# Kernel optimization log

Measured on AMD Instinct MI355X. Metric: run time of the kernel, lower is better.

Reference implementation:

```python
import jax, jax.numpy as jnp
import numpy as np

NU, NI, E = 20000, 8000, 64
DV, DT = 4096, 768
NE, B = 200000, 4096
L_HET, L_HOMO = 2, 1
K_ISG, K_UCG = 10, 20
MMW, WD = 0.1, 1e-4


def setup_inputs() -> dict:
    ks = jax.random.split(jax.random.key(0), 14)
    return {
        "feat_v": jax.random.normal(ks[0], (NI, DV), jnp.float32),
        "feat_t": jax.random.normal(ks[1], (NI, DT), jnp.float32),
        "pref_v": jax.random.normal(ks[2], (NU, E), jnp.float32) * 0.1,
        "pref_t": jax.random.normal(ks[3], (NU, E), jnp.float32) * 0.1,
        "W_v": jax.random.normal(ks[4], (DV, E), jnp.float32) * 0.02,
        "W_t": jax.random.normal(ks[5], (DT, E), jnp.float32) * 0.02,
        "user_v_alpha": jax.random.normal(ks[6], (1,), jnp.float32),
        "user_nb_weights": jax.random.normal(ks[7], (NU, K_UCG), jnp.float32),
        "edge_users": jax.random.randint(ks[8], (NE,), 0, NU, jnp.int32),
        "edge_items": jax.random.randint(ks[9], (NE,), 0, NI, jnp.int32),
        "u_ids": jax.random.randint(ks[10], (B,), 0, NU, jnp.int32),
        "pos_ids": jax.random.randint(ks[11], (B,), 0, NI, jnp.int32),
        "neg_ids": jax.random.randint(ks[12], (B,), 0, NI, jnp.int32),
        "user_nb": jax.random.randint(ks[13], (NU, K_UCG), 0, NU, jnp.int32),
    }


def reference(feat_v, feat_t, pref_v, pref_t, W_v, W_t, user_v_alpha,
              user_nb_weights, edge_users, edge_items, u_ids, pos_ids,
              neg_ids, user_nb):
    N = NU + NI
    # bidirectional bipartite edges (items offset by NU)
    src = jnp.concatenate([edge_users, edge_items + NU])
    dst = jnp.concatenate([edge_items + NU, edge_users])
    deg = jax.ops.segment_sum(jnp.ones_like(src, jnp.float32), dst, num_segments=N)
    deg = jnp.maximum(deg, 1.0)
    norm = (1.0 / jnp.sqrt(deg[src] * deg[dst]))[:, None]

    def hetero_gcn(feat, pref, W):
        x = jnp.concatenate([pref, feat @ W], axis=0)  # [N, E]
        h, out = x, x
        for _ in range(L_HET):
            h = jax.ops.segment_sum(h[src] * norm, dst, num_segments=N)
            out = out + h
        return out[:NU], out[NU:]

    u_v, i_v = hetero_gcn(feat_v, pref_v, W_v)
    u_t, i_t = hetero_gcn(feat_t, pref_t, W_t)
    a_v = jax.nn.sigmoid(user_v_alpha[0])
    u_f = jnp.concatenate([a_v * u_v, (1.0 - a_v) * u_t], axis=1)  # [NU, 2E]
    i_f = jnp.concatenate([i_v, i_t], axis=1)                      # [NI, 2E]

    # Item Semantic Graph: KNN over cosine sim, no grad through adjacency.
    def knn_adj(f):
        fn = f / jnp.linalg.norm(f, axis=-1, keepdims=True)
        sim = fn @ fn.T                       # [NI, NI]
        _, idx = jax.lax.top_k(sim, K_ISG)
        return jnp.zeros((NI, NI), f.dtype).at[jnp.arange(NI)[:, None], idx].set(1.0)

    adj = jax.lax.stop_gradient(MMW * knn_adj(feat_v) + (1.0 - MMW) * knn_adj(feat_t))
    rs = adj.sum(axis=1)
    adj = adj * jnp.where(rs > 0, 1.0 / rs, 0.0)[:, None]

    h_i = i_f
    for _ in range(L_HOMO):
        h_i = adj @ h_i

    # User Co-occurrence Graph: scatter-softmax attention aggregation, vectorized.
    attn = jax.nn.softmax(user_nb_weights, axis=1)  # [NU, K]
    h_u = u_f
    for _ in range(L_HOMO):
        h_u = jnp.einsum('uk,ukd->ud', attn, h_u[user_nb])

    z_u = u_f + h_u
    z_i = i_f + h_i
    pos = jnp.sum(z_u[u_ids] * z_i[pos_ids], axis=1)
    neg = jnp.sum(z_u[u_ids] * z_i[neg_ids], axis=1)
    bpr = -jnp.mean(jax.nn.log_sigmoid(pos - neg))
    reg = WD * (jnp.sum(pref_v ** 2) + jnp.sum(pref_t ** 2) + user_v_alpha[0] ** 2) / 2.0
    return bpr + reg
```

## Files before the change

### kernel.cpp

```cpp
#include <hip/hip_runtime.h>
#include <cstdint>
#include <cstddef>

#define NU_C   20000
#define NI_C   8000
#define NTOT_C 28000
#define NE_C   200000
#define B_C    4096
#define NPAD_C 8064
#define NCHUNK 63
#define NPAIR  2016

typedef unsigned short u16;
typedef unsigned int   u32;
typedef unsigned char  u8;
typedef __bf16 bf16x8 __attribute__((ext_vector_type(8)));
typedef float  f32x4  __attribute__((ext_vector_type(4)));

static __device__ __forceinline__ u16 f2bf(float f) {
  u32 u = __float_as_uint(f);
  return (u16)((u + 0x7fffu + ((u >> 16) & 1u)) >> 16);
}

static __device__ __forceinline__ void gl_lds16(const void* g, void* l) {
  __builtin_amdgcn_global_load_lds(
      (const __attribute__((address_space(1))) void*)g,
      (__attribute__((address_space(3))) void*)l, 16, 0, 0);
}

static __device__ __forceinline__ int xcd_swz(int b) {
  return (b & 7) * (NPAIR / 8) + (b >> 3);
}

__global__ void conv_kernel2(const float* __restrict__ Fv, const float* __restrict__ Ft,
                             u16* __restrict__ Fbv, u16* __restrict__ Fbt,
                             u8* __restrict__ Fv8,
                             float* __restrict__ rnv, float* __restrict__ rnt,
                             const float* __restrict__ pv, const float* __restrict__ pt,
                             float* __restrict__ x2) {
  int b = blockIdx.x;
  const int tid = threadIdx.x;
  float ss = 0.f;
  if (b < NPAD_C) {
    const int row = b;
    u16* dst  = Fbv + (size_t)row * 4096;
    u8*  dst8 = Fv8 + (size_t)row * 4096;
    if (row < NI_C) {
      const float* src = Fv + (size_t)row * 4096;
      for (int c = tid * 4; c < 4096; c += 1024) {
        float4 f = *(const float4*)(src + c);
        ss += f.x*f.x + f.y*f.y + f.z*f.z + f.w*f.w;
        ushort4 v; v.x = f2bf(f.x); v.y = f2bf(f.y); v.z = f2bf(f.z); v.w = f2bf(f.w);
        *(ushort4*)(dst + c) = v;
        int w8 = __builtin_amdgcn_cvt_pk_fp8_f32(f.x, f.y, 0, false);
        w8 = __builtin_amdgcn_cvt_pk_fp8_f32(f.z, f.w, w8, true);
        *(u32*)(dst8 + c) = (u32)w8;
      }
    } else {
      for (int c = tid * 4; c < 4096; c += 1024) {
        ushort4 v; v.x = v.y = v.z = v.w = 0;
        *(ushort4*)(dst + c) = v;
        *(u32*)(dst8 + c) = 0u;
      }
    }
    #pragma unroll
    for (int off = 32; off; off >>= 1) ss += __shfl_xor(ss, off);
    __shared__ float red[4];
    if ((tid & 63) == 0) red[tid >> 6] = ss;
    __syncthreads();
    if (tid == 0) {
      float s = red[0] + red[1] + red[2] + red[3];
      rnv[row] = (row < NI_C) ? rsqrtf(s) : 0.f;
    }
  } else if (b < 2 * NPAD_C) {
    const int row = b - NPAD_C;
    u16* dst = Fbt + (size_t)row * 768;
    if (row < NI_C) {
      const float* src = Ft + (size_t)row * 768;
      for (int c = tid * 4; c < 768; c += 1024) {
        float4 f = *(const float4*)(src + c);
        ss += f.x*f.x + f.y*f.y + f.z*f.z + f.w*f.w;
        ushort4 v; v.x = f2bf(f.x); v.y = f2bf(f.y); v.z = f2bf(f.z); v.w = f2bf(f.w);
        *(ushort4*)(dst + c) = v;
      }
    } else {
      for (int c = tid * 4; c < 768; c += 1024) {
        ushort4 v; v.x = v.y = v.z = v.w = 0;
        *(ushort4*)(dst + c) = v;
      }
    }
    #pragma unroll
    for (int off = 32; off; off >>= 1) ss += __shfl_xor(ss, off);
    __shared__ float red[4];
    if ((tid & 63) == 0) red[tid >> 6] = ss;
    __syncthreads();
    if (tid == 0) {
      float s = red[0] + red[1] + red[2] + red[3];
      rnt[row] = (row < NI_C) ? rsqrtf(s) : 0.f;
    }
  } else {
    const int b2 = b - 2 * NPAD_C;
    #pragma unroll
    for (int k = 0; k < 8; ++k) {
      int gid = b2 * 2048 + k * 256 + tid;
      int u = gid >> 7, c = gid & 127;
      x2[gid] = (c < 64) ? pv[(size_t)u * 64 + c] : pt[(size_t)u * 64 + (c - 64)];
    }
  }
}

static __device__ __forceinline__ void simtopk_fp8_body(
    int bid, char* smem, const u8* __restrict__ F, const float* __restrict__ rn,
    u32* __restrict__ tv) {
  u8*    sB   = (u8*)smem;
  u8*    sA   = (u8*)(smem + 16384);
  float* T    = (float*)smem;
  int*   mk   = (int*)smem;
  int*   mk2  = (int*)(smem + 20480);
  float* sRNI = (float*)(smem + 33792);
  float* sRNJ = (float*)(smem + 34304);

  const int tid  = threadIdx.x;
  const int lane = tid & 63;
  const int wv   = tid >> 6;
  const int n15  = lane & 15;
  const int quad = lane >> 4;

  int I = 0, rem = xcd_swz(bid);
  { int rowlen = NCHUNK;
    while (rem >= rowlen) { rem -= rowlen; rowlen--; I++; } }
  const int J = I + rem;

  const int l2   = lane >> 2;
  const int lseg = (lane & 3) ^ (l2 & 3) ^ (lane >> 4);
  const u8* gB[2]; const u8* gA[2]; u8* lB[2]; u8* lA[2];
  #pragma unroll
  for (int rep = 0; rep < 2; ++rep) {
    int row = wv * 32 + rep * 16 + l2;
    gB[rep] = F + (size_t)(I * 128 + row) * 4096 + lseg * 16;
    gA[rep] = F + (size_t)(J * 128 + row) * 4096 + lseg * 16;
    lB[rep] = sB + (wv * 32 + rep * 16) * 64;
    lA[rep] = sA + (wv * 32 + rep * 16) * 64;
  }
  const int s_n = (n15 & 3) ^ (n15 >> 2);
  const int q2  = quad >> 1;
  const int q8  = (quad & 1) * 8;
  const int rB0 = (wv * 32 + n15) * 64;
  const int rB1 = rB0 + 16 * 64;

  f32x4 acc[2][8];
  #pragma unroll
  for (int tf = 0; tf < 2; ++tf)
    #pragma unroll
    for (int af = 0; af < 8; ++af) { f32x4 z = {0.f,0.f,0.f,0.f}; acc[tf][af] = z; }

  for (int k0 = 0; k0 < 4096; k0 += 128) {
    __syncthreads();
    gl_lds16(gB[0] + k0,      lB[0]);
    gl_lds16(gB[0] + k0 + 64, lB[0] + 8192);
    gl_lds16(gB[1] + k0,      lB[1]);
    gl_lds16(gB[1] + k0 + 64, lB[1] + 8192);
    gl_lds16(gA[0] + k0,      lA[0]);
    gl_lds16(gA[0] + k0 + 64, lA[0] + 8192);
    gl_lds16(gA[1] + k0,      lA[1]);
    gl_lds16(gA[1] + k0 + 64, lA[1] + 8192);
    if (k0 == 0) {
      if (tid < 128) sRNJ[tid] = rn[J * 128 + tid];
      else           sRNI[tid - 128] = rn[I * 128 + (tid - 128)];
    }
    __syncthreads();
    #pragma unroll
    for (int ksub = 0; ksub < 2; ++ksub) {
      const u8* bBase = sB + ksub * 8192;
      const u8* aBase = sA + ksub * 8192;
      #pragma unroll
      for (int ks = 0; ks < 2; ++ks) {
        const int sw = (((ks * 2 + q2) ^ s_n) << 4) + q8;
        long long b0 = *(const long long*)(bBase + rB0 + sw);
        long long b1 = *(const long long*)(bBase + rB1 + sw);
        #pragma unroll
        for (int af = 0; af < 8; ++af) {
          long long a = *(const long long*)(aBase + (af * 16 + n15) * 64 + sw);
          acc[0][af] = __builtin_amdgcn_mfma_f32_16x16x32_fp8_fp8(a, b0, acc[0][af], 0, 0, 0);
          acc[1][af] = __builtin_amdgcn_mfma_f32_16x16x32_fp8_fp8(a, b1, acc[1][af], 0, 0, 0);
        }
      }
    }
  }

  int bk[2][10];
  #pragma unroll
  for (int tf = 0; tf < 2; ++tf)
    #pragma unroll
    for (int j = 0; j < 10; ++j) bk[tf][j] = 0;

  #pragma unroll
  for (int af = 0; af < 8; ++af) {
    const float4 rn4 = *(const float4*)(sRNJ + af * 16 + quad * 4);
    const float rna[4] = {rn4.x, rn4.y, rn4.z, rn4.w};
    #pragma unroll
    for (int r = 0; r < 4; ++r) {
      const int ci = J * 128 + af * 16 + quad * 4 + r;
      #pragma unroll
      for (int tf = 0; tf < 2; ++tf) {
        float v = acc[tf][af][r] * rna[r];
        int key = (int)((__float_as_uint(v) & 0xFFFFE000u) | (u32)ci);
        if (ci < NI_C && key > bk[tf][9]) {
          bk[tf][9] = key;
          #pragma unroll
          for (int j = 9; j > 0; --j)
            if (bk[tf][j] > bk[tf][j-1]) { int t = bk[tf][j]; bk[tf][j] = bk[tf][j-1]; bk[tf][j-1] = t; }
        }
      }
    }
  }
  __syncthreads();
  #pragma unroll
  for (int tf = 0; tf < 2; ++tf) {
    int rl = wv * 32 + tf * 16 + n15;
    #pragma unroll
    for (int j = 0; j < 10; ++j) mk[rl * 40 + quad * 10 + j] = bk[tf][j];
  }
  __syncthreads();
  if (tid < 128) {
    int* m = mk + tid * 40;
    int h0 = 0, h1 = 10, h2 = 20, h3 = 30;
    int v0 = m[0], v1 = m[10], v2 = m[20], v3 = m[30];
    #pragma unroll
    for (int s = 0; s < 10; ++s) {
      int m01 = v0 > v1 ? v0 : v1, m23 = v2 > v3 ? v2 : v3;
      int mx = m01 > m23 ? m01 : m23;
      mk2[tid * 10 + s] = mx;
      if      (mx == v0) { ++h0; v0 = (h0 < 10) ? m[h0] : (int)0x80000000; }
      else if (mx == v1) { ++h1; v1 = (h1 < 20) ? m[h1] : (int)0x80000000; }
      else if (mx == v2) { ++h2; v2 = (h2 < 30) ? m[h2] : (int)0x80000000; }
      else               { ++h3; v3 = (h3 < 40) ? m[h3] : (int)0x80000000; }
    }
  }
  __syncthreads();
  { u32* o = tv + ((size_t)J * NPAD_C + I * 128) * 10;
    for (int g = tid; g < 1280; g += 256) o[g] = (u32)mk2[g]; }

  if (I == J) return;

  int bj[2][10];
  #pragma unroll
  for (int s = 0; s < 2; ++s)
    #pragma unroll
    for (int j = 0; j < 10; ++j) bj[s][j] = 0;

  #pragma unroll
  for (int tf = 0; tf < 2; ++tf) {
    __syncthreads();
    #pragma unroll
    for (int af = 0; af < 8; ++af)
      #pragma unroll
      for (int r = 0; r < 4; ++r)
        T[(af * 16 + quad * 4 + r) * 66 + wv * 16 + n15] = acc[tf][af][r];
    __syncthreads();
    #pragma unroll
    for (int s = 0; s < 2; ++s) {
      const int c_own = wv * 32 + s * 16 + n15;
      #pragma unroll
      for (int j = 0; j < 16; ++j) {
        const int t  = quad * 32 + tf * 16 + j;
        const int t64 = quad * 16 + j;
        float v = T[c_own * 66 + t64] * sRNI[t];
        const int ti = I * 128 + t;
        int key = (int)((__float_as_uint(v) & 0xFFFFE000u) | (u32)ti);
        if (ti < NI_C && key > bj[s][9]) {
          bj[s][9] = key;
          #pragma unroll
          for (int q = 9; q > 0; --q)
            if (bj[s][q] > bj[s][q-1]) { int tt = bj[s][q]; bj[s][q] = bj[s][q-1]; bj[s][q-1] = tt; }
        }
      }
    }
  }
  __syncthreads();
  #pragma unroll
  for (int s = 0; s < 2; ++s) {
    int rl = wv * 32 + s * 16 + n15;
    #pragma unroll
    for (int j = 0; j < 10; ++j) mk[rl * 40 + quad * 10 + j] = bj[s][j];
  }
  __syncthreads();
  if (tid < 128) {
    int* m = mk + tid * 40;
    int h0 = 0, h1 = 10, h2 = 20, h3 = 30;
    int v0 = m[0], v1 = m[10], v2 = m[20], v3 = m[30];
    #pragma unroll
    for (int s = 0; s < 10; ++s) {
      int m01 = v0 > v1 ? v0 : v1, m23 = v2 > v3 ? v2 : v3;
      int mx = m01 > m23 ? m01 : m23;
      mk2[tid * 10 + s] = mx;
      if      (mx == v0) { ++h0; v0 = (h0 < 10) ? m[h0] : (int)0x80000000; }
      else if (mx == v1) { ++h1; v1 = (h1 < 20) ? m[h1] : (int)0x80000000; }
      else if (mx == v2) { ++h2; v2 = (h2 < 30) ? m[h2] : (int)0x80000000; }
      else               { ++h3; v3 = (h3 < 40) ? m[h3] : (int)0x80000000; }
    }
  }
  __syncthreads();
  { u32* o = tv + ((size_t)I * NPAD_C + J * 128) * 10;
    for (int g = tid; g < 1280; g += 256) o[g] = (u32)mk2[g]; }
}

static __device__ __forceinline__ void simtopk_bf16_body(
    int bid, char* smem, const u16* __restrict__ F, const float* __restrict__ rn,
    u32* __restrict__ tv) {
  u16*   sB   = (u16*)smem;
  u16*   sA   = (u16*)(smem + 16384);
  float* T    = (float*)smem;
  int*   mk   = (int*)smem;
  int*   mk2  = (int*)(smem + 20480);
  float* sRNI = (float*)(smem + 34816);
  float* sRNJ = (float*)(smem + 35328);

  const int tid  = threadIdx.x;
  const int lane = tid & 63;
  const int wv   = tid >> 6;
  const int n15  = lane & 15;
  const int quad = lane >> 4;

  int I = 0, rem = xcd_swz(bid);
  { int rowlen = NCHUNK;
    while (rem >= rowlen) { rem -= rowlen; rowlen--; I++; } }
  const int J = I + rem;

  const int l8  = lane >> 3;
  const int sgu = ((lane & 7) ^ l8) << 3;
  const u16* gB[4]; const u16* gA[4]; u16* lB[4]; u16* lA[4];
  #pragma unroll
  for (int rep = 0; rep < 4; ++rep) {
    int row = wv * 32 + rep * 8 + l8;
    gB[rep] = F + (size_t)(I * 128 + row) * 768 + sgu;
    gA[rep] = F + (size_t)(J * 128 + row) * 768 + sgu;
    lB[rep] = sB + wv * 2048 + rep * 512;
    lA[rep] = sA + wv * 2048 + rep * 512;
  }
  const int swu0 = ((quad    ) ^ (n15 & 7)) << 3;
  const int swu1 = ((quad + 4) ^ (n15 & 7)) << 3;
  const int rowB0 = (wv * 32 + n15) * 64;
  const int rowB1 = rowB0 + 16 * 64;

  f32x4 acc[2][8];
  #pragma unroll
  for (int tf = 0; tf < 2; ++tf)
    #pragma unroll
    for (int af = 0; af < 8; ++af) { f32x4 z = {0.f,0.f,0.f,0.f}; acc[tf][af] = z; }

  for (int k0 = 0; k0 < 768; k0 += 64) {
    __syncthreads();
    #pragma unroll
    for (int rep = 0; rep < 4; ++rep) gl_lds16(gB[rep] + k0, lB[rep]);
    #pragma unroll
    for (int rep = 0; rep < 4; ++rep) gl_lds16(gA[rep] + k0, lA[rep]);
    if (k0 == 0) {
      if (tid < 128) sRNJ[tid] = rn[J * 128 + tid];
      else           sRNI[tid - 128] = rn[I * 128 + (tid - 128)];
    }
    __syncthreads();
    #pragma unroll
    for (int ks = 0; ks < 2; ++ks) {
      const int swu = ks ? swu1 : swu0;
      bf16x8 b0 = *(const bf16x8*)(sB + rowB0 + swu);
      bf16x8 b1 = *(const bf16x8*)(sB + rowB1 + swu);
      #pragma unroll
      for (int af = 0; af < 8; ++af) {
        bf16x8 a = *(const bf16x8*)(sA + (af * 16 + n15) * 64 + swu);
        acc[0][af] = __builtin_amdgcn_mfma_f32_16x16x32_bf16(a, b0, acc[0][af], 0, 0, 0);
        acc[1][af] = __builtin_amdgcn_mfma_f32_16x16x32_bf16(a, b1, acc[1][af], 0, 0, 0);
      }
    }
  }

  int bk[2][10];
  #pragma unroll
  for (int tf = 0; tf < 2; ++tf)
    #pragma unroll
    for (int j = 0; j < 10; ++j) bk[tf][j] = 0;

  #pragma unroll
  for (int af = 0; af < 8; ++af) {
    const float4 rn4 = *(const float4*)(sRNJ + af * 16 + quad * 4);
    const float rna[4] = {rn4.x, rn4.y, rn4.z, rn4.w};
    #pragma unroll
    for (int r = 0; r < 4; ++r) {
      const int ci = J * 128 + af * 16 + quad * 4 + r;
      #pragma unroll
      for (int tf = 0; tf < 2; ++tf) {
        float v = acc[tf][af][r] * rna[r];
        int key = (int)((__float_as_uint(v) & 0xFFFFE000u) | (u32)ci);
        if (ci < NI_C && key > bk[tf][9]) {
          bk[tf][9] = key;
          #pragma unroll
          for (int j = 9; j > 0; --j)
            if (bk[tf][j] > bk[tf][j-1]) { int t = bk[tf][j]; bk[tf][j] = bk[tf][j-1]; bk[tf][j-1] = t; }
        }
      }
    }
  }
  __syncthreads();
  #pragma unroll
  for (int tf = 0; tf < 2; ++tf) {
    int rl = wv * 32 + tf * 16 + n15;
    #pragma unroll
    for (int j = 0; j < 10; ++j) mk[rl * 40 + quad * 10 + j] = bk[tf][j];
  }
  __syncthreads();
  if (tid < 128) {
    int* m = mk + tid * 40;
    int h0 = 0, h1 = 10, h2 = 20, h3 = 30;
    int v0 = m[0], v1 = m[10], v2 = m[20], v3 = m[30];
    #pragma unroll
    for (int s = 0; s < 10; ++s) {
      int m01 = v0 > v1 ? v0 : v1, m23 = v2 > v3 ? v2 : v3;
      int mx = m01 > m23 ? m01 : m23;
      mk2[tid * 10 + s] = mx;
      if      (mx == v0) { ++h0; v0 = (h0 < 10) ? m[h0] : (int)0x80000000; }
      else if (mx == v1) { ++h1; v1 = (h1 < 20) ? m[h1] : (int)0x80000000; }
      else if (mx == v2) { ++h2; v2 = (h2 < 30) ? m[h2] : (int)0x80000000; }
      else               { ++h3; v3 = (h3 < 40) ? m[h3] : (int)0x80000000; }
    }
  }
  __syncthreads();
  { u32* o = tv + ((size_t)J * NPAD_C + I * 128) * 10;
    for (int g = tid; g < 1280; g += 256) o[g] = (u32)mk2[g]; }

  if (I == J) return;

  int bj[2][10];
  #pragma unroll
  for (int s = 0; s < 2; ++s)
    #pragma unroll
    for (int j = 0; j < 10; ++j) bj[s][j] = 0;

  #pragma unroll
  for (int tf = 0; tf < 2; ++tf) {
    __syncthreads();
    #pragma unroll
    for (int af = 0; af < 8; ++af)
      #pragma unroll
      for (int r = 0; r < 4; ++r)
        T[(af * 16 + quad * 4 + r) * 66 + wv * 16 + n15] = acc[tf][af][r];
    __syncthreads();
    #pragma unroll
    for (int s = 0; s < 2; ++s) {
      const int c_own = wv * 32 + s * 16 + n15;
      #pragma unroll
      for (int j = 0; j < 16; ++j) {
        const int t  = quad * 32 + tf * 16 + j;
        const int t64 = quad * 16 + j;
        float v = T[c_own * 66 + t64] * sRNI[t];
        const int ti = I * 128 + t;
        int key = (int)((__float_as_uint(v) & 0xFFFFE000u) | (u32)ti);
        if (ti < NI_C && key > bj[s][9]) {
          bj[s][9] = key;
          #pragma unroll
          for (int q = 9; q > 0; --q)
            if (bj[s][q] > bj[s][q-1]) { int tt = bj[s][q]; bj[s][q] = bj[s][q-1]; bj[s][q-1] = tt; }
        }
      }
    }
  }
  __syncthreads();
  #pragma unroll
  for (int s = 0; s < 2; ++s) {
    int rl = wv * 32 + s * 16 + n15;
    #pragma unroll
    for (int j = 0; j < 10; ++j) mk[rl * 40 + quad * 10 + j] = bj[s][j];
  }
  __syncthreads();
  if (tid < 128) {
    int* m = mk + tid * 40;
    int h0 = 0, h1 = 10, h2 = 20, h3 = 30;
    int v0 = m[0], v1 = m[10], v2 = m[20], v3 = m[30];
    #pragma unroll
    for (int s = 0; s < 10; ++s) {
      int m01 = v0 > v1 ? v0 : v1, m23 = v2 > v3 ? v2 : v3;
      int mx = m01 > m23 ? m01 : m23;
      mk2[tid * 10 + s] = mx;
      if      (mx == v0) { ++h0; v0 = (h0 < 10) ? m[h0] : (int)0x80000000; }
      else if (mx == v1) { ++h1; v1 = (h1 < 20) ? m[h1] : (int)0x80000000; }
      else if (mx == v2) { ++h2; v2 = (h2 < 30) ? m[h2] : (int)0x80000000; }
      else               { ++h3; v3 = (h3 < 40) ? m[h3] : (int)0x80000000; }
    }
  }
  __syncthreads();
  { u32* o = tv + ((size_t)I * NPAD_C + J * 128) * 10;
    for (int g = tid; g < 1280; g += 256) o[g] = (u32)mk2[g]; }
}

static __device__ __forceinline__ void merge4_body(int mb, int* fkbase,
                                                   const u32* __restrict__ tv,
                                                   int* __restrict__ idx) {
  const int w    = threadIdx.x >> 6;
  const int lane = threadIdx.x & 63;
  const int row  = mb * 4 + w;
  int* fk = fkbase + w * 640;
  for (int g = lane; g < 630; g += 64)
    fk[g] = (int)tv[((size_t)(g / 10) * NPAD_C + row) * 10 + (g % 10)];
  if (lane < 10) fk[630 + lane] = (int)0x80000000;
  __syncthreads();
  int v[10];
  #pragma unroll
  for (int j = 0; j < 10; ++j) v[j] = fk[lane + j * 64];
  #pragma unroll 1
  for (int s = 0; s < 10; ++s) {
    int loc = v[0];
    #pragma unroll
    for (int j = 1; j < 10; ++j) loc = v[j] > loc ? v[j] : loc;
    #pragma unroll
    for (int off = 32; off; off >>= 1) {
      int o = __shfl_xor(loc, off); loc = o > loc ? o : loc;
    }
    if (lane == 0) idx[row * 10 + s] = loc & 0x1FFF;
    #pragma unroll
    for (int j = 0; j < 10; ++j) if (v[j] == loc) v[j] = (int)0x80000000;
  }
}

__launch_bounds__(256)
__global__ void merge4_kernel(const u32* __restrict__ tv, int* __restrict__ idx) {
  __shared__ int fk[4 * 640];
  merge4_body(blockIdx.x, fk, tv, idx);
}

template<int D>
static __device__ __forceinline__ void gemm_xw_body(
    int bid, char* smem, const u16* __restrict__ F, const u16* __restrict__ Wt,
    float* __restrict__ x2, int modeoff) {
  u16* sF = (u16*)smem;
  const int tid  = threadIdx.x;
  const int lane = tid & 63;
  const int wv   = tid >> 6;
  const int n15  = lane & 15;
  const int quad = lane >> 4;
  const int l8   = lane >> 3;
  const int sgu  = ((lane & 7) ^ l8) << 3;
  const u16* gF[2]; u16* lF[2];
  #pragma unroll
  for (int rep = 0; rep < 2; ++rep) {
    int row = rep * 32 + wv * 8 + l8;
    gF[rep] = F + (size_t)(bid * 64 + row) * D + sgu;
    lF[rep] = sF + (rep * 32 + wv * 8) * 64;
  }
  const int swu0 = ((quad    ) ^ (n15 & 7)) << 3;
  const int swu1 = ((quad + 4) ^ (n15 & 7)) << 3;

  f32x4 acc[4];
  #pragma unroll
  for (int nf = 0; nf < 4; ++nf) { f32x4 z = {0.f,0.f,0.f,0.f}; acc[nf] = z; }

  for (int k0 = 0; k0 < D; k0 += 64) {
    __syncthreads();
    gl_lds16(gF[0] + k0, lF[0]);
    gl_lds16(gF[1] + k0, lF[1]);
    __syncthreads();
    #pragma unroll
    for (int ks = 0; ks < 2; ++ks) {
      const int swu = ks ? swu1 : swu0;
      bf16x8 a = *(const bf16x8*)(sF + (wv * 16 + n15) * 64 + swu);
      #pragma unroll
      for (int nf = 0; nf < 4; ++nf) {
        bf16x8 b = *(const bf16x8*)(Wt + (size_t)(nf * 16 + n15) * D + k0 + ks * 32 + quad * 8);
        acc[nf] = __builtin_amdgcn_mfma_f32_16x16x32_bf16(a, b, acc[nf], 0, 0, 0);
      }
    }
  }
  #pragma unroll
  for (int nf = 0; nf < 4; ++nf)
    #pragma unroll
    for (int r = 0; r < 4; ++r) {
      int row = bid * 64 + wv * 16 + quad * 4 + r;
      if (row < NI_C)
        x2[(size_t)(NU_C + row) * 128 + modeoff + nf * 16 + n15] = acc[nf][r];
    }
}

static __device__ __forceinline__ void gather2_body(
    int bid, const int* __restrict__ row_start, const int* __restrict__ esrc,
    const float* __restrict__ ew, const float* __restrict__ x2, float* __restrict__ h1) {
  const int node = bid * 2 + (threadIdx.x >> 7);
  const int ch   = threadIdx.x & 127;
  if (node >= NTOT_C) return;
  const int b = row_start[node], e = row_start[node + 1];
  float acc = 0.f;
  for (int i = b; i < e; ++i)
    acc += ew[i] * x2[(size_t)esrc[i] * 128 + ch];
  h1[(size_t)node * 128 + ch] = acc;
}

static __device__ __forceinline__ void gather_comb2_body(
    int bid, const int* __restrict__ row_start, const int* __restrict__ esrc,
    const float* __restrict__ ew, const float* __restrict__ x2,
    const float* __restrict__ h1, const float* __restrict__ alpha,
    float* __restrict__ uf, float* __restrict__ ifb) {
  const int node = bid * 2 + (threadIdx.x >> 7);
  const int ch   = threadIdx.x & 127;
  if (node >= NTOT_C) return;
  const int b = row_start[node], e = row_start[node + 1];
  float acc = 0.f;
  for (int i = b; i < e; ++i)
    acc += ew[i] * h1[(size_t)esrc[i] * 128 + ch];
  float val = x2[(size_t)node * 128 + ch] + h1[(size_t)node * 128 + ch] + acc;
  if (node < NU_C) {
    float av = 1.f / (1.f + expf(-alpha[0]));
    float coef = (ch < 64) ? av : (1.f - av);
    uf[(size_t)node * 128 + ch] = coef * val;
  } else {
    ifb[(size_t)(node - NU_C) * 128 + ch] = val;
  }
}

__launch_bounds__(256)
__global__ void fusedA_kernel(const u8* __restrict__ F8, const float* __restrict__ rnv,
                              u32* __restrict__ tv,
                              const u16* __restrict__ Fvb, const u16* __restrict__ Wtv,
                              const u16* __restrict__ Ftb, const u16* __restrict__ Wtt,
                              float* __restrict__ x2) {
  __shared__ __align__(16) char smem[34816];
  int b = blockIdx.x;
  if (b < 125) { gemm_xw_body<4096>(b, smem, Fvb, Wtv, x2, 0); return; }
  b -= 125;
  if (b < 125) { gemm_xw_body<768>(b, smem, Ftb, Wtt, x2, 64); return; }
  simtopk_fp8_body(b - 125, smem, F8, rnv, tv);
}

__launch_bounds__(256)
__global__ void fusedB_kernel(const int* __restrict__ row_start, const int* __restrict__ esrc,
                              const float* __restrict__ ew, const float* __restrict__ x2,
                              float* __restrict__ h1,
                              const u32* __restrict__ tv, int* __restrict__ idx) {
  __shared__ int fk[4 * 640];
  int b = blockIdx.x;
  if (b < 2000) { merge4_body(b, fk, tv, idx); return; }
  gather2_body(b - 2000, row_start, esrc, ew, x2, h1);
}

__launch_bounds__(256)
__global__ void fusedC_kernel(const u16* __restrict__ Ftb, const float* __restrict__ rnt,
                              u32* __restrict__ tv2,
                              const int* __restrict__ row_start, const int* __restrict__ esrc,
                              const float* __restrict__ ew, const float* __restrict__ x2,
                              const float* __restrict__ h1, const float* __restrict__ alpha,
                              float* __restrict__ uf, float* __restrict__ ifb) {
  __shared__ __align__(16) char smem[40960];
  int b = blockIdx.x;
  if (b < NPAIR) { simtopk_bf16_body(b, smem, Ftb, rnt, tv2); return; }
  gather_comb2_body(b - NPAIR, row_start, esrc, ew, x2, h1, alpha, uf, ifb);
}

__global__ void deg_count_kernel(const int* __restrict__ eu, const int* __restrict__ ei,
                                 float* deg) {
  int e = blockIdx.x * 256 + threadIdx.x;
  if (e < NE_C) {
    atomicAdd(&deg[eu[e]], 1.f);
    atomicAdd(&deg[NU_C + ei[e]], 1.f);
  }
}

__global__ void scan_kernel(float* __restrict__ deg, int* __restrict__ row_start,
                            int* __restrict__ cursor) {
  __shared__ int part[1024];
  const int tid = threadIdx.x;
  const int base = tid * 28;
  float dl[28];
  int local[28];
  int s = 0;
  #pragma unroll
  for (int j = 0; j < 28; ++j) {
    int n = base + j;
    float df = (n < NTOT_C) ? deg[n] : 0.f;
    dl[j] = df;
    local[j] = s; s += (int)df;
  }
  part[tid] = s;
  __syncthreads();
  for (int off = 1; off < 1024; off <<= 1) {
    int v = (tid >= off) ? part[tid - off] : 0;
    __syncthreads();
    part[tid] += v;
    __syncthreads();
  }
  int pre = (tid > 0) ? part[tid - 1] : 0;
  #pragma unroll
  for (int j = 0; j < 28; ++j) {
    int n = base + j;
    if (n < NTOT_C) {
      row_start[n] = pre + local[j];
      cursor[n]    = pre + local[j];
      deg[n]       = rsqrtf(fmaxf(dl[j], 1.f));
    }
  }
  if (tid == 1023) row_start[NTOT_C] = part[1023];
}

__global__ void place_kernel(const int* __restrict__ eu, const int* __restrict__ ei,
                             const float* __restrict__ dinv, int* __restrict__ cursor,
                             int* __restrict__ esrc, float* __restrict__ ew) {
  int e = blockIdx.x * 256 + threadIdx.x;
  if (e >= NE_C) return;
  int u = eu[e], v = NU_C + ei[e];
  float w = dinv[u] * dinv[v];
  int p1 = atomicAdd(&cursor[v], 1);  esrc[p1] = u; ew[p1] = w;
  int p2 = atomicAdd(&cursor[u], 1);  esrc[p2] = v; ew[p2] = w;
}

__global__ void wtrans_kernel(const float* __restrict__ Wv, const float* __restrict__ Wti,
                              u16* __restrict__ Ov, u16* __restrict__ Ot) {
  __shared__ u16 sT[64][72];
  int b = blockIdx.x;
  const float* W; u16* O; int D;
  if (b < 64) { W = Wv; O = Ov; D = 4096; }
  else        { b -= 64; W = Wti; O = Ot; D = 768; }
  const int k0 = b * 64;
  const int r = threadIdx.x >> 6;
  const int c = threadIdx.x & 63;
  for (int rr = r; rr < 64; rr += 4)
    sT[c][rr] = f2bf(W[(size_t)(k0 + rr) * 64 + c]);
  __syncthreads();
  const int n = threadIdx.x >> 2, seg = threadIdx.x & 3;
  uint4 a0 = *(const uint4*)&sT[n][seg * 16];
  uint4 a1 = *(const uint4*)&sT[n][seg * 16 + 8];
  *(uint4*)(O + (size_t)n * D + k0 + seg * 16)     = a0;
  *(uint4*)(O + (size_t)n * D + k0 + seg * 16 + 8) = a1;
}

__global__ void zuzi_kernel(const float* __restrict__ uf, const float* __restrict__ w,
                            const int* __restrict__ nb, const float* __restrict__ ifb,
                            const int* __restrict__ iv, const int* __restrict__ it,
                            float* __restrict__ zu, float* __restrict__ zi) {
  const int c = threadIdx.x;
  if (blockIdx.x < NU_C) {
    const int u = blockIdx.x;
    __shared__ float at[20];
    if (c < 20) at[c] = w[u * 20 + c];
    __syncthreads();
    float e[20]; float m = -1e30f;
    #pragma unroll
    for (int k = 0; k < 20; ++k) { e[k] = at[k]; m = fmaxf(m, e[k]); }
    float ssum = 0.f;
    #pragma unroll
    for (int k = 0; k < 20; ++k) { e[k] = expf(e[k] - m); ssum += e[k]; }
    float inv = 1.f / ssum;
    float acc = 0.f;
    #pragma unroll
    for (int k = 0; k < 20; ++k) {
      int j = nb[u * 20 + k];
      acc += e[k] * inv * uf[(size_t)j * 128 + c];
    }
    zu[(size_t)u * 128 + c] = uf[(size_t)u * 128 + c] + acc;
  } else {
    const int i = blockIdx.x - NU_C;
    float sv = 0.f, st = 0.f;
    #pragma unroll
    for (int k = 0; k < 10; ++k) sv += ifb[(size_t)iv[i * 10 + k] * 128 + c];
    #pragma unroll
    for (int k = 0; k < 10; ++k) st += ifb[(size_t)it[i * 10 + k] * 128 + c];
    zi[(size_t)i * 128 + c] = ifb[(size_t)i * 128 + c] + 0.01f * sv + 0.09f * st;
  }
}

__global__ void loss_kernel(const float* __restrict__ zu, const float* __restrict__ zi,
                            const int* __restrict__ uid, const int* __restrict__ pid,
                            const int* __restrict__ nid, const float* __restrict__ pv,
                            const float* __restrict__ pt, const float* __restrict__ alpha,
                            float* __restrict__ out) {
  if (blockIdx.x < 1024) {
    int wv = threadIdx.x >> 6, lane = threadIdx.x & 63;
    int b = blockIdx.x * 4 + wv;
    int u = uid[b], p = pid[b], n = nid[b];
    float2 a  = *(const float2*)(zu + (size_t)u * 128 + lane * 2);
    float2 xp = *(const float2*)(zi + (size_t)p * 128 + lane * 2);
    float2 xn = *(const float2*)(zi + (size_t)n * 128 + lane * 2);
    float d = a.x * (xp.x - xn.x) + a.y * (xp.y - xn.y);
    #pragma unroll
    for (int off = 32; off; off >>= 1) d += __shfl_xor(d, off);
    if (lane == 0) {
      float xv = -d;
      float sp = fmaxf(xv, 0.f) + log1pf(expf(-fabsf(xv)));
      atomicAdd(out, sp * (1.f / (float)B_C));
    }
  } else {
    const size_t N1 = (size_t)NU_C * 64;
    float acc = 0.f;
    for (size_t i = (size_t)(blockIdx.x - 1024) * 256 + threadIdx.x; i < 2 * N1;
         i += (size_t)512 * 256) {
      float x = (i < N1) ? pv[i] : pt[i - N1];
      acc += x * x;
    }
    #pragma unroll
    for (int off = 32; off; off >>= 1) acc += __shfl_xor(acc, off);
    __shared__ float red[4];
    if ((threadIdx.x & 63) == 0) red[threadIdx.x >> 6] = acc;
    __syncthreads();
    if (threadIdx.x == 0) {
      float s = red[0] + red[1] + red[2] + red[3];
      atomicAdd(out, 0.5e-4f * s);
    }
    if (blockIdx.x == 1024 && threadIdx.x == 0) {
      float a = alpha[0];
      atomicAdd(out, 0.5e-4f * a * a);
    }
  }
}

extern "C" void kernel_launch(void* const* d_in, const int* in_sizes, int n_in,
                              void* d_out, int out_size, void* d_ws, size_t ws_size,
                              hipStream_t stream) {
  const float* feat_v = (const float*)d_in[0];
  const float* feat_t = (const float*)d_in[1];
  const float* pref_v = (const float*)d_in[2];
  const float* pref_t = (const float*)d_in[3];
  const float* W_v    = (const float*)d_in[4];
  const float* W_t    = (const float*)d_in[5];
  const float* alpha  = (const float*)d_in[6];
  const float* unw    = (const float*)d_in[7];
  const int* eu       = (const int*)d_in[8];
  const int* ei       = (const int*)d_in[9];
  const int* u_ids    = (const int*)d_in[10];
  const int* pos_ids  = (const int*)d_in[11];
  const int* neg_ids  = (const int*)d_in[12];
  const int* user_nb  = (const int*)d_in[13];
  float* out = (float*)d_out;
  char* ws = (char*)d_ws;

  size_t off = 0;
  auto alloc = [&](size_t bytes) { char* p = ws + off; off += (bytes + 255) & ~(size_t)255; return p; };
  u16*   fvbf  = (u16*)alloc((size_t)NPAD_C * 4096 * 2);
  u8*    fv8   = (u8*)alloc((size_t)NPAD_C * 4096);
  u16*   ftbf  = (u16*)alloc((size_t)NPAD_C * 768 * 2);
  u16*   wtv   = (u16*)alloc((size_t)64 * 4096 * 2);
  u16*   wtt   = (u16*)alloc((size_t)64 * 768 * 2);
  float* rn_v  = (float*)alloc(NPAD_C * 4);
  float* rn_t  = (float*)alloc(NPAD_C * 4);
  int*   idx_v = (int*)alloc(NI_C * 10 * 4);
  int*   idx_t = (int*)alloc(NI_C * 10 * 4);
  float* dinv  = (float*)alloc(NTOT_C * 4);
  int*   rowst = (int*)alloc((NTOT_C + 1) * 4);
  int*   curs  = (int*)alloc(NTOT_C * 4);
  int*   esrc  = (int*)alloc((size_t)2 * NE_C * 4);
  float* ew    = (float*)alloc((size_t)2 * NE_C * 4);
  float* x2    = (float*)alloc((size_t)NTOT_C * 128 * 4);
  float* h1    = (float*)alloc((size_t)NTOT_C * 128 * 4);
  char*  pC    = alloc((size_t)(NU_C + NI_C) * 128 * 4 * 2);
  u32*   tvb   = (u32*)pC;
  u32*   tvb2  = (u32*)fvbf;
  float* u_f   = (float*)pC;
  float* i_f   = (float*)(pC + (size_t)NU_C * 128 * 4);
  float* z_u   = (float*)(pC + (size_t)(NU_C + NI_C) * 128 * 4);
  float* z_i   = (float*)(pC + (size_t)(2 * NU_C + NI_C) * 128 * 4);

  hipMemsetAsync(out, 0, sizeof(float), stream);
  hipMemsetAsync(dinv, 0, NTOT_C * 4, stream);

  deg_count_kernel<<<(NE_C + 255) / 256, 256, 0, stream>>>(eu, ei, dinv);
  scan_kernel<<<1, 1024, 0, stream>>>(dinv, rowst, curs);
  place_kernel<<<(NE_C + 255) / 256, 256, 0, stream>>>(eu, ei, dinv, curs, esrc, ew);
  conv_kernel2<<<2 * NPAD_C + 1250, 256, 0, stream>>>(feat_v, feat_t, fvbf, ftbf, fv8,
                                                      rn_v, rn_t, pref_v, pref_t, x2);
  wtrans_kernel<<<76, 256, 0, stream>>>(W_v, W_t, wtv, wtt);

  fusedA_kernel<<<250 + NPAIR, 256, 0, stream>>>(
      fv8, rn_v, tvb, fvbf, wtv, ftbf, wtt, x2);

  fusedB_kernel<<<2000 + 14000, 256, 0, stream>>>(rowst, esrc, ew, x2, h1, tvb, idx_v);

  fusedC_kernel<<<NPAIR + 14000, 256, 0, stream>>>(
      ftbf, rn_t, tvb2, rowst, esrc, ew, x2, h1, alpha, u_f, i_f);

  merge4_kernel<<<2000, 256, 0, stream>>>(tvb2, idx_t);
  zuzi_kernel<<<NU_C + NI_C, 128, 0, stream>>>(u_f, unw, user_nb, i_f, idx_v, idx_t, z_u, z_i);
  loss_kernel<<<1536, 256, 0, stream>>>(z_u, z_i, u_ids, pos_ids, neg_ids,
                                        pref_v, pref_t, alpha, out);
}
```

Before: 1.048 ms.

## Reschedule stages into fewer fused launches to overlap independent work

Folds degree counting and the weight transpose into the conversion kernel, and folds CSR placement into fusedA. The bf16 similarity top-k moves from fusedC up into fusedB, alongside the visual merge and the first gather. The text merge moves into fusedC, so the standalone merge kernel is removed. This cuts the number of kernel launches and lets independent stages share a grid to fill idle CUs. The cost is heavier multi-role kernels and more careful reasoning about buffer aliasing (tvb2 reuses the fvbf region) across the new stage order.

```diff
diff --git a/kernel.cpp b/kernel.cpp
--- a/kernel.cpp
+++ b/kernel.cpp
@@ -32,12 +32,36 @@
   return (b & 7) * (NPAIR / 8) + (b >> 3);
 }
 
+static __device__ __forceinline__ void wtrans_body(int b, const float* __restrict__ Wv,
+                                                   const float* __restrict__ Wti,
+                                                   u16* __restrict__ Ov, u16* __restrict__ Ot) {
+  __shared__ u16 sT[64][72];
+  const float* W; u16* O; int D;
+  if (b < 64) { W = Wv; O = Ov; D = 4096; }
+  else        { b -= 64; W = Wti; O = Ot; D = 768; }
+  const int k0 = b * 64;
+  const int r = threadIdx.x >> 6;
+  const int c = threadIdx.x & 63;
+  for (int rr = r; rr < 64; rr += 4)
+    sT[c][rr] = f2bf(W[(size_t)(k0 + rr) * 64 + c]);
+  __syncthreads();
+  const int n = threadIdx.x >> 2, seg = threadIdx.x & 3;
+  uint4 a0 = *(const uint4*)&sT[n][seg * 16];
+  uint4 a1 = *(const uint4*)&sT[n][seg * 16 + 8];
+  *(uint4*)(O + (size_t)n * D + k0 + seg * 16)     = a0;
+  *(uint4*)(O + (size_t)n * D + k0 + seg * 16 + 8) = a1;
+}
+
 __global__ void conv_kernel2(const float* __restrict__ Fv, const float* __restrict__ Ft,
                              u16* __restrict__ Fbv, u16* __restrict__ Fbt,
                              u8* __restrict__ Fv8,
                              float* __restrict__ rnv, float* __restrict__ rnt,
                              const float* __restrict__ pv, const float* __restrict__ pt,
-                             float* __restrict__ x2) {
+                             float* __restrict__ x2,
+                             const float* __restrict__ Wv, const float* __restrict__ Wti,
+                             u16* __restrict__ wtv, u16* __restrict__ wtt,
+                             const int* __restrict__ eu, const int* __restrict__ ei,
+                             float* __restrict__ deg) {
   int b = blockIdx.x;
   const int tid = threadIdx.x;
   float ss = 0.f;
@@ -98,13 +122,22 @@
       float s = red[0] + red[1] + red[2] + red[3];
       rnt[row] = (row < NI_C) ? rsqrtf(s) : 0.f;
     }
-  } else {
-    const int b2 = b - 2 * NPAD_C;
+  } else if (b < 2 * NPAD_C + 76) {
+    wtrans_body(b - 2 * NPAD_C, Wv, Wti, wtv, wtt);
+  } else if (b < 2 * NPAD_C + 76 + 1250) {
+    const int b2 = b - (2 * NPAD_C + 76);
     #pragma unroll
     for (int k = 0; k < 8; ++k) {
       int gid = b2 * 2048 + k * 256 + tid;
       int u = gid >> 7, c = gid & 127;
       x2[gid] = (c < 64) ? pv[(size_t)u * 64 + c] : pt[(size_t)u * 64 + (c - 64)];
+    }
+  } else {
+    const int b2 = b - (2 * NPAD_C + 76 + 1250);
+    int e = b2 * 256 + tid;
+    if (e < NE_C) {
+      atomicAdd(&deg[eu[e]], 1.f);
+      atomicAdd(&deg[NU_C + ei[e]], 1.f);
     }
   }
 }
@@ -518,12 +551,6 @@
     #pragma unroll
     for (int j = 0; j < 10; ++j) if (v[j] == loc) v[j] = (int)0x80000000;
   }
-}
-
-__launch_bounds__(256)
-__global__ void merge4_kernel(const u32* __restrict__ tv, int* __restrict__ idx) {
-  __shared__ int fk[4 * 640];
-  merge4_body(blockIdx.x, fk, tv, idx);
 }
 
 template<int D>
@@ -613,51 +640,62 @@
   }
 }
 
+static __device__ __forceinline__ void place_body(
+    int bid, const int* __restrict__ eu, const int* __restrict__ ei,
+    const float* __restrict__ dinv, int* __restrict__ cursor,
+    int* __restrict__ esrc, float* __restrict__ ew) {
+  int e = bid * 256 + threadIdx.x;
+  if (e >= NE_C) return;
+  int u = eu[e], v = NU_C + ei[e];
+  float w = dinv[u] * dinv[v];
+  int p1 = atomicAdd(&cursor[v], 1);  esrc[p1] = u; ew[p1] = w;
+  int p2 = atomicAdd(&cursor[u], 1);  esrc[p2] = v; ew[p2] = w;
+}
+
 __launch_bounds__(256)
 __global__ void fusedA_kernel(const u8* __restrict__ F8, const float* __restrict__ rnv,
                               u32* __restrict__ tv,
                               const u16* __restrict__ Fvb, const u16* __restrict__ Wtv,
                               const u16* __restrict__ Ftb, const u16* __restrict__ Wtt,
-                              float* __restrict__ x2) {
+                              float* __restrict__ x2,
+                              const int* __restrict__ eu, const int* __restrict__ ei,
+                              const float* __restrict__ dinv, int* __restrict__ cursor,
+                              int* __restrict__ esrc, float* __restrict__ ew) {
   __shared__ __align__(16) char smem[34816];
   int b = blockIdx.x;
   if (b < 125) { gemm_xw_body<4096>(b, smem, Fvb, Wtv, x2, 0); return; }
   b -= 125;
   if (b < 125) { gemm_xw_body<768>(b, smem, Ftb, Wtt, x2, 64); return; }
-  simtopk_fp8_body(b - 125, smem, F8, rnv, tv);
+  b -= 125;
+  if (b < NPAIR) { simtopk_fp8_body(b, smem, F8, rnv, tv); return; }
+  place_body(b - NPAIR, eu, ei, dinv, cursor, esrc, ew);
 }
 
 __launch_bounds__(256)
-__global__ void fusedB_kernel(const int* __restrict__ row_start, const int* __restrict__ esrc,
+__global__ void fusedB_kernel(const u16* __restrict__ Ftb, const float* __restrict__ rnt,
+                              u32* __restrict__ tv2,
+                              const u32* __restrict__ tv, int* __restrict__ idx,
+                              const int* __restrict__ row_start, const int* __restrict__ esrc,
                               const float* __restrict__ ew, const float* __restrict__ x2,
-                              float* __restrict__ h1,
-                              const u32* __restrict__ tv, int* __restrict__ idx) {
-  __shared__ int fk[4 * 640];
+                              float* __restrict__ h1) {
+  __shared__ __align__(16) char smem[40960];
   int b = blockIdx.x;
-  if (b < 2000) { merge4_body(b, fk, tv, idx); return; }
+  if (b < NPAIR) { simtopk_bf16_body(b, smem, Ftb, rnt, tv2); return; }
+  b -= NPAIR;
+  if (b < 2000) { merge4_body(b, (int*)smem, tv, idx); return; }
   gather2_body(b - 2000, row_start, esrc, ew, x2, h1);
 }
 
 __launch_bounds__(256)
-__global__ void fusedC_kernel(const u16* __restrict__ Ftb, const float* __restrict__ rnt,
-                              u32* __restrict__ tv2,
+__global__ void fusedC_kernel(const u32* __restrict__ tv2, int* __restrict__ idxt,
                               const int* __restrict__ row_start, const int* __restrict__ esrc,
                               const float* __restrict__ ew, const float* __restrict__ x2,
                               const float* __restrict__ h1, const float* __restrict__ alpha,
                               float* __restrict__ uf, float* __restrict__ ifb) {
-  __shared__ __align__(16) char smem[40960];
+  __shared__ __align__(16) int fk[4 * 640];
   int b = blockIdx.x;
-  if (b < NPAIR) { simtopk_bf16_body(b, smem, Ftb, rnt, tv2); return; }
-  gather_comb2_body(b - NPAIR, row_start, esrc, ew, x2, h1, alpha, uf, ifb);
-}
-
-__global__ void deg_count_kernel(const int* __restrict__ eu, const int* __restrict__ ei,
-                                 float* deg) {
-  int e = blockIdx.x * 256 + threadIdx.x;
-  if (e < NE_C) {
-    atomicAdd(&deg[eu[e]], 1.f);
-    atomicAdd(&deg[NU_C + ei[e]], 1.f);
-  }
+  if (b < 2000) { merge4_body(b, fk, tv2, idxt); return; }
+  gather_comb2_body(b - 2000, row_start, esrc, ew, x2, h1, alpha, uf, ifb);
 }
 
 __global__ void scan_kernel(float* __restrict__ deg, int* __restrict__ row_start,
@@ -694,37 +732,6 @@
     }
   }
   if (tid == 1023) row_start[NTOT_C] = part[1023];
-}
-
-__global__ void place_kernel(const int* __restrict__ eu, const int* __restrict__ ei,
-                             const float* __restrict__ dinv, int* __restrict__ cursor,
-                             int* __restrict__ esrc, float* __restrict__ ew) {
-  int e = blockIdx.x * 256 + threadIdx.x;
-  if (e >= NE_C) return;
-  int u = eu[e], v = NU_C + ei[e];
-  float w = dinv[u] * dinv[v];
-  int p1 = atomicAdd(&cursor[v], 1);  esrc[p1] = u; ew[p1] = w;
-  int p2 = atomicAdd(&cursor[u], 1);  esrc[p2] = v; ew[p2] = w;
-}
-
-__global__ void wtrans_kernel(const float* __restrict__ Wv, const float* __restrict__ Wti,
-                              u16* __restrict__ Ov, u16* __restrict__ Ot) {
-  __shared__ u16 sT[64][72];
-  int b = blockIdx.x;
-  const float* W; u16* O; int D;
-  if (b < 64) { W = Wv; O = Ov; D = 4096; }
-  else        { b -= 64; W = Wti; O = Ot; D = 768; }
-  const int k0 = b * 64;
-  const int r = threadIdx.x >> 6;
-  const int c = threadIdx.x & 63;
-  for (int rr = r; rr < 64; rr += 4)
-    sT[c][rr] = f2bf(W[(size_t)(k0 + rr) * 64 + c]);
-  __syncthreads();
-  const int n = threadIdx.x >> 2, seg = threadIdx.x & 3;
-  uint4 a0 = *(const uint4*)&sT[n][seg * 16];
-  uint4 a1 = *(const uint4*)&sT[n][seg * 16 + 8];
-  *(uint4*)(O + (size_t)n * D + k0 + seg * 16)     = a0;
-  *(uint4*)(O + (size_t)n * D + k0 + seg * 16 + 8) = a1;
 }
 
 __global__ void zuzi_kernel(const float* __restrict__ uf, const float* __restrict__ w,
@@ -855,22 +862,21 @@
   hipMemsetAsync(out, 0, sizeof(float), stream);
   hipMemsetAsync(dinv, 0, NTOT_C * 4, stream);
 
-  deg_count_kernel<<<(NE_C + 255) / 256, 256, 0, stream>>>(eu, ei, dinv);
+  conv_kernel2<<<2 * NPAD_C + 76 + 1250 + (NE_C + 255) / 256, 256, 0, stream>>>(
+      feat_v, feat_t, fvbf, ftbf, fv8, rn_v, rn_t, pref_v, pref_t, x2,
+      W_v, W_t, wtv, wtt, eu, ei, dinv);
+
   scan_kernel<<<1, 1024, 0, stream>>>(dinv, rowst, curs);
-  place_kernel<<<(NE_C + 255) / 256, 256, 0, stream>>>(eu, ei, dinv, curs, esrc, ew);
-  conv_kernel2<<<2 * NPAD_C + 1250, 256, 0, stream>>>(feat_v, feat_t, fvbf, ftbf, fv8,
-                                                      rn_v, rn_t, pref_v, pref_t, x2);
-  wtrans_kernel<<<76, 256, 0, stream>>>(W_v, W_t, wtv, wtt);
-
-  fusedA_kernel<<<250 + NPAIR, 256, 0, stream>>>(
-      fv8, rn_v, tvb, fvbf, wtv, ftbf, wtt, x2);
-
-  fusedB_kernel<<<2000 + 14000, 256, 0, stream>>>(rowst, esrc, ew, x2, h1, tvb, idx_v);
-
-  fusedC_kernel<<<NPAIR + 14000, 256, 0, stream>>>(
-      ftbf, rn_t, tvb2, rowst, esrc, ew, x2, h1, alpha, u_f, i_f);
-
-  merge4_kernel<<<2000, 256, 0, stream>>>(tvb2, idx_t);
+
+  fusedA_kernel<<<250 + NPAIR + (NE_C + 255) / 256, 256, 0, stream>>>(
+      fv8, rn_v, tvb, fvbf, wtv, ftbf, wtt, x2, eu, ei, dinv, curs, esrc, ew);
+
+  fusedB_kernel<<<NPAIR + 2000 + 14000, 256, 0, stream>>>(
+      ftbf, rn_t, tvb2, tvb, idx_v, rowst, esrc, ew, x2, h1);
+
+  fusedC_kernel<<<2000 + 14000, 256, 0, stream>>>(
+      tvb2, idx_t, rowst, esrc, ew, x2, h1, alpha, u_f, i_f);
+
   zuzi_kernel<<<NU_C + NI_C, 128, 0, stream>>>(u_f, unw, user_nb, i_f, idx_v, idx_t, z_u, z_i);
   loss_kernel<<<1536, 256, 0, stream>>>(z_u, z_i, u_ids, pos_ids, neg_ids,
                                         pref_v, pref_t, alpha, out);
```

New measurement: 1.004 ms. 1.04x faster.
